# Kernel optimization log

Measured on AMD Instinct MI355X. Metric: run time of the kernel, lower is better.

## Reference

```python
import jax, jax.numpy as jnp
import numpy as np

HID = 384
KV = 384
HEADS = 2
LAYERS = 2
KFFN = 9
WIN = 0.2
SIGMA = 0.3
EPS = 1e-5
HDIM = HID // HEADS


def _sin_pos(T, dim):
    # fairseq SinusoidalPositionalEmbedding; inputs are nonzero floats so all
    # positions are "non-pad": positions = arange(T) + padding_idx + 1 = 1..T
    pos = jnp.arange(1, T + 1, dtype=jnp.float32)
    half = dim // 2
    freqs = jnp.exp(-np.log(10000.0) / (half - 1) * jnp.arange(half, dtype=jnp.float32))
    ang = pos[:, None] * freqs[None, :]
    return jnp.concatenate([jnp.sin(ang), jnp.cos(ang)], axis=-1)  # [T, dim]


def _ln(x, g, b):
    m = jnp.mean(x, axis=-1, keepdims=True)
    v = jnp.var(x, axis=-1, keepdims=True)
    return (x - m) * jax.lax.rsqrt(v + EPS) * g + b


def _window_mask(T1, T2):
    # per-query sliding window over keys (vectorized form of the Python loop)
    w = int(T2 * WIN) // 2
    t = jnp.arange(T1)
    c = (t * T2) // T1                      # win_center = int(t/T1*T2)
    lo = jnp.maximum(0, c - w)
    j = jnp.arange(T2)
    allowed = (j[None, :] >= lo[:, None]) & (j[None, :] < (c + w)[:, None])
    return ~allowed                          # True = masked out, [T1, T2]


def _forward(x1, x2, pos_alpha, ln1_g, ln1_b, qw, kw, vw, ow,
             ln2_g, ln2_b, cw, cb, lw, lb, lnf_g, lnf_b):
    B, T1, C = x1.shape
    T2 = x2.shape[1]
    # no padding (random-normal inputs never have zero abs-sum rows), so all
    # nonpadding multiplies are identity and key_padding_mask is a no-op.
    x1 = x1 + pos_alpha * _sin_pos(T1, C)[None]
    x2 = x2 + pos_alpha * _sin_pos(T2, KV)[None]

    mask = _window_mask(T1, T2)              # [T1, T2] bool
    scaling = HDIM ** -0.5
    guided_loss = jnp.float32(0.0)
    # guided attention mask (lengths == full lengths, no padding)
    ti = jnp.arange(T1, dtype=jnp.float32)[:, None] / T1
    sj = jnp.arange(T2, dtype=jnp.float32)[None, :] / T2
    gmask = 1.0 - jnp.exp(-((sj - ti) ** 2) / (2.0 * SIGMA ** 2))  # [T1, T2]

    aw = None
    for i in range(LAYERS):
        residual = x1
        qn = _ln(x1, ln1_g[i], ln1_b[i])
        q = jnp.einsum('btc,dc->btd', qn, qw[i]) * scaling
        k = jnp.einsum('bsc,dc->bsd', x2, kw[i])
        v = jnp.einsum('bsc,dc->bsd', x2, vw[i])
        q = q.reshape(B, T1, HEADS, HDIM)
        k = k.reshape(B, T2, HEADS, HDIM)
        v = v.reshape(B, T2, HEADS, HDIM)
        scores = jnp.einsum('bqhd,bkhd->bhqk', q, k)
        scores = jnp.where(mask[None, None], jnp.float32(-1e9), scores)
        p = jax.nn.softmax(scores, axis=-1)                  # [B,H,T1,T2]
        attn = jnp.einsum('bhqk,bkhd->bqhd', p, v).reshape(B, T1, C)
        attn = jnp.einsum('btc,dc->btd', attn, ow[i])
        x1 = residual + attn
        if i == 0:  # num_guided_layers = 1
            aw = p.mean(axis=1)                              # head-avg [B,T1,T2]
            guided_loss = guided_loss + (aw * gmask[None]).mean()
        # FFN: Conv1d(C->4C, k=9, SAME) * k^-0.5 -> gelu -> Linear(4C->C)
        residual = x1
        y = _ln(x1, ln2_g[i], ln2_b[i])
        yt = jnp.transpose(y, (0, 2, 1))                     # [B,C,T1]
        h = jax.lax.conv_general_dilated(yt, cw[i], (1,), 'SAME',
                                         dimension_numbers=('NCH', 'OIH', 'NCH'))
        h = (h + cb[i][None, :, None]) * (KFFN ** -0.5)
        h = jax.nn.gelu(jnp.transpose(h, (0, 2, 1)), approximate=False)  # [B,T1,4C]
        y = jnp.einsum('btf,cf->btc', h, lw[i]) + lb[i]
        x1 = residual + y

    x1 = _ln(x1, lnf_g, lnf_b)
    return x1, guided_loss


def setup_inputs() -> dict:
    key = jax.random.key(0)
    ks = jax.random.split(key, 16)
    s = 0.02
    B, T1, T2 = 8, 2048, 512
    return {
        'x1': jax.random.normal(ks[0], (B, T1, HID), jnp.float32),
        'x2': jax.random.normal(ks[1], (B, T2, KV), jnp.float32),
        'pos_alpha': jnp.float32(1.0),
        'ln1_g': jnp.ones((LAYERS, HID), jnp.float32),
        'ln1_b': jnp.zeros((LAYERS, HID), jnp.float32),
        'qw': jax.random.normal(ks[2], (LAYERS, HID, HID), jnp.float32) * s,
        'kw': jax.random.normal(ks[3], (LAYERS, HID, KV), jnp.float32) * s,
        'vw': jax.random.normal(ks[4], (LAYERS, HID, KV), jnp.float32) * s,
        'ow': jax.random.normal(ks[5], (LAYERS, HID, HID), jnp.float32) * s,
        'ln2_g': jnp.ones((LAYERS, HID), jnp.float32),
        'ln2_b': jnp.zeros((LAYERS, HID), jnp.float32),
        'cw': jax.random.normal(ks[6], (LAYERS, 4 * HID, HID, KFFN), jnp.float32) * s,
        'cb': jnp.zeros((LAYERS, 4 * HID), jnp.float32),
        'lw': jax.random.normal(ks[7], (LAYERS, HID, 4 * HID), jnp.float32) * s,
        'lb': jnp.zeros((LAYERS, HID), jnp.float32),
        'lnf_g': jnp.ones((HID,), jnp.float32),
        'lnf_b': jnp.zeros((HID,), jnp.float32),
    }


def reference(x1, x2, pos_alpha, ln1_g, ln1_b, qw, kw, vw, ow,
              ln2_g, ln2_b, cw, cb, lw, lb, lnf_g, lnf_b):
    return _forward(x1, x2, pos_alpha, ln1_g, ln1_b, qw, kw, vw, ow,
                    ln2_g, ln2_b, cw, cb, lw, lb, lnf_g, lnf_b)
```

## Files before the change

### kernel.cpp

```cpp
#include <hip/hip_runtime.h>
#include <math.h>

#define NB 8
#define NT1 2048
#define NT2 512
#define NC 384
#define ND 192
#define NF 1536
#define NKI 3456
#define TPAD 2056

typedef __attribute__((ext_vector_type(8))) short bf16x8;
typedef __attribute__((ext_vector_type(4))) float f32x4;

#define GLOAD16(gsrc, ldst) \
  __builtin_amdgcn_global_load_lds((const __attribute__((address_space(1))) void*)(gsrc), \
                                   (__attribute__((address_space(3))) void*)(ldst), 16, 0, 0)

static __device__ __forceinline__ unsigned short f2bf(float f) {
  unsigned int u = __float_as_uint(f);
  unsigned int r = (u + 0x7fffu + ((u >> 16) & 1u)) >> 16;
  return (unsigned short)r;
}

static __device__ __forceinline__ float warp_sum(float v) {
#pragma unroll
  for (int off = 32; off > 0; off >>= 1) v += __shfl_xor(v, off);
  return v;
}

__global__ __launch_bounds__(256) void k_add_pos2(const float* __restrict__ x,
    const float* __restrict__ alpha_p, float* __restrict__ y, int T, int total2) {
  int i = blockIdx.x * 256 + threadIdx.x;
  if (i >= total2) return;
  int j = i % 192;
  int row = i / 192;
  int t = row % T;
  float freq = __expf(-0.0482216773f * (float)j);
  float ang = (float)(t + 1) * freq;
  float sn, cs;
  __sincosf(ang, &sn, &cs);
  float a = alpha_p[0];
  size_t base = (size_t)row * NC;
  y[base + j] = x[base + j] + a * sn;
  y[base + j + 192] = x[base + j + 192] + a * cs;
}

__global__ __launch_bounds__(256) void k_add_pos2_bf16(const float* __restrict__ x,
    const float* __restrict__ alpha_p, unsigned short* __restrict__ y, int T, int total2) {
  int i = blockIdx.x * 256 + threadIdx.x;
  if (i >= total2) return;
  int j = i % 192;
  int row = i / 192;
  int t = row % T;
  float freq = __expf(-0.0482216773f * (float)j);
  float ang = (float)(t + 1) * freq;
  float sn, cs;
  __sincosf(ang, &sn, &cs);
  float a = alpha_p[0];
  size_t base = (size_t)row * NC;
  y[base + j] = f2bf(x[base + j] + a * sn);
  y[base + j + 192] = f2bf(x[base + j + 192] + a * cs);
}

__global__ __launch_bounds__(256) void k_ln(const float* __restrict__ x,
    const float* __restrict__ g, const float* __restrict__ b,
    float* __restrict__ y, int nrows) {
  int row = blockIdx.x * 4 + (threadIdx.x >> 6);
  int lane = threadIdx.x & 63;
  if (row >= nrows) return;
  const float* xr = x + (size_t)row * NC;
  float v[6];
  float s = 0.f, s2 = 0.f;
#pragma unroll
  for (int i = 0; i < 6; ++i) {
    float t = xr[lane + 64 * i];
    v[i] = t; s += t; s2 += t * t;
  }
  s = warp_sum(s); s2 = warp_sum(s2);
  float mean = s * (1.f / NC);
  float var = s2 * (1.f / NC) - mean * mean;
  float rs = rsqrtf(var + 1e-5f);
  float* yr = y + (size_t)row * NC;
#pragma unroll
  for (int i = 0; i < 6; ++i) {
    int cc = lane + 64 * i;
    yr[cc] = (v[i] - mean) * rs * g[cc] + b[cc];
  }
}

__global__ __launch_bounds__(256) void k_ln_bf16(const float* __restrict__ x,
    const float* __restrict__ g, const float* __restrict__ b,
    unsigned short* __restrict__ y) {
  int row = blockIdx.x * 4 + (threadIdx.x >> 6);
  int lane = threadIdx.x & 63;
  const float* xr = x + (size_t)row * NC;
  float v[6];
  float s = 0.f, s2 = 0.f;
#pragma unroll
  for (int i = 0; i < 6; ++i) {
    float t = xr[lane + 64 * i];
    v[i] = t; s += t; s2 += t * t;
  }
  s = warp_sum(s); s2 = warp_sum(s2);
  float mean = s * (1.f / NC);
  float var = s2 * (1.f / NC) - mean * mean;
  float rs = rsqrtf(var + 1e-5f);
  unsigned short* yr = y + (size_t)row * NC;
#pragma unroll
  for (int i = 0; i < 6; ++i) {
    int cc = lane + 64 * i;
    yr[cc] = f2bf((v[i] - mean) * rs * g[cc] + b[cc]);
  }
}

__global__ __launch_bounds__(256) void k_ln_bf16p(const float* __restrict__ x,
    const float* __restrict__ g, const float* __restrict__ b,
    unsigned short* __restrict__ ypad) {
  int row = blockIdx.x * 4 + (threadIdx.x >> 6);
  int lane = threadIdx.x & 63;
  const float* xr = x + (size_t)row * NC;
  float v[6];
  float s = 0.f, s2 = 0.f;
#pragma unroll
  for (int i = 0; i < 6; ++i) {
    float t = xr[lane + 64 * i];
    v[i] = t; s += t; s2 += t * t;
  }
  s = warp_sum(s); s2 = warp_sum(s2);
  float mean = s * (1.f / NC);
  float var = s2 * (1.f / NC) - mean * mean;
  float rs = rsqrtf(var + 1e-5f);
  int bb = row >> 11, t = row & 2047;
  unsigned short* yr = ypad + ((size_t)(bb * TPAD + t + 4)) * NC;
#pragma unroll
  for (int i = 0; i < 6; ++i) {
    int cc = lane + 64 * i;
    yr[cc] = f2bf((v[i] - mean) * rs * g[cc] + b[cc]);
  }
}

__global__ __launch_bounds__(256) void k_zero_guard(unsigned short* __restrict__ ypad) {
  int i = blockIdx.x * 256 + threadIdx.x;
  if (i >= 24576) return;
  int c = i % NC;
  int r = (i / NC) % 8;
  int b = i / (NC * 8);
  int t = (r < 4) ? r : (2048 + r);
  ypad[((size_t)b * TPAD + t) * NC + c] = 0;
}

__global__ __launch_bounds__(256) void k_pack_cw2(const float* __restrict__ cw,
    unsigned short* __restrict__ cwp) {
  __shared__ float s[NKI];
  int f = blockIdx.x;
  const float* src = cw + (size_t)f * NKI;
  for (int i = threadIdx.x; i < NKI; i += 256) s[i] = src[i];
  __syncthreads();
  unsigned short* dst = cwp + (size_t)f * NKI;
  for (int i = threadIdx.x; i < NKI; i += 256) {
    int kk = i / NC, cc = i - kk * NC;
    dst[i] = f2bf(s[cc * 9 + kk]);
  }
}

__global__ __launch_bounds__(256) void k_cvt_qkvo(const float* __restrict__ qw,
    const float* __restrict__ kw, const float* __restrict__ vw,
    const float* __restrict__ ow, unsigned short* __restrict__ dst, float qscale) {
  int i = blockIdx.x * 256 + threadIdx.x;
  if (i >= 4 * 294912) return;
  int w = i / 294912;
  int j = i - w * 294912;
  const float* s = (w == 0) ? qw : (w == 1) ? kw : (w == 2) ? vw : ow;
  float sc = (w == 0) ? qscale : 1.f;
  dst[i] = f2bf(s[j] * sc);
}

__global__ __launch_bounds__(256) void k_cvt(const float* __restrict__ x,
    unsigned short* __restrict__ y, int n) {
  int i = blockIdx.x * 256 + threadIdx.x;
  if (i < n) y[i] = f2bf(x[i]);
}

__global__ __launch_bounds__(256) void k_pgemm_qkv(
    const unsigned short* __restrict__ Aq,
    const unsigned short* __restrict__ Akv,
    const unsigned short* __restrict__ Wq,
    const unsigned short* __restrict__ Wk,
    const unsigned short* __restrict__ Wv,
    unsigned short* __restrict__ Qb,
    unsigned short* __restrict__ Kb,
    unsigned short* __restrict__ Vtb) {
  __shared__ unsigned short As[128 * 32];
  __shared__ unsigned short Bs[128 * 32];
  const int y = blockIdx.y;
  const int which = (y < 128) ? 0 : (y < 160) ? 1 : 2;
  const unsigned short* A = (which == 0) ? Aq : Akv;
  const unsigned short* W = (which == 0) ? Wq : (which == 1) ? Wk : Wv;
  const int bm = ((which == 0) ? y : (which == 1) ? (y - 128) : (y - 160)) * 128;
  const int bn = blockIdx.x * 128;
  const int tid = threadIdx.x;
  const int lane = tid & 63, wv = tid >> 6;
  const int wr = (wv >> 1) * 64, wc = (wv & 1) * 64;
  f32x4 acc[4][4] = {};

  const int chunk = wv * 2;
  const int rloc = chunk * 16 + (lane >> 2);
  const int slot = (lane & 3) << 3;
  const size_t abase = ((size_t)(bm + rloc)) * NC + slot;
  const size_t bbase = ((size_t)(bn + rloc)) * NC + slot;
  unsigned short* AsW0 = &As[chunk * 512];
  unsigned short* AsW1 = &As[(chunk + 1) * 512];
  unsigned short* BsW0 = &Bs[chunk * 512];
  unsigned short* BsW1 = &Bs[(chunk + 1) * 512];

  const int rsel = lane & 15, ksel = (lane >> 4) * 8;

  for (int kt = 0; kt < NC; kt += 32) {
    GLOAD16(A + abase + kt, AsW0);
    GLOAD16(A + abase + kt + (size_t)16 * NC, AsW1);
    GLOAD16(W + bbase + kt, BsW0);
    GLOAD16(W + bbase + kt + (size_t)16 * NC, BsW1);
    __syncthreads();
    bf16x8 af[4], bfr[4];
#pragma unroll
    for (int m = 0; m < 4; ++m)
      af[m] = *(const bf16x8*)&As[(wr + m * 16 + rsel) * 32 + ksel];
#pragma unroll
    for (int n = 0; n < 4; ++n)
      bfr[n] = *(const bf16x8*)&Bs[(wc + n * 16 + rsel) * 32 + ksel];
#pragma unroll
    for (int m = 0; m < 4; ++m)
#pragma unroll
      for (int n = 0; n < 4; ++n)
        acc[m][n] = __builtin_amdgcn_mfma_f32_16x16x32_bf16(af[m], bfr[n], acc[m][n], 0, 0, 0);
    __syncthreads();
  }

  const int col0 = bn + wc + (lane & 15);
  const int row0 = bm + wr + (lane >> 4) * 4;
#pragma unroll
  for (int m = 0; m < 4; ++m) {
#pragma unroll
    for (int n = 0; n < 4; ++n) {
      int col = col0 + n * 16;
#pragma unroll
      for (int r = 0; r < 4; ++r) {
        int row = row0 + m * 16 + r;
        unsigned short bv = f2bf(acc[m][n][r]);
        if (which == 0) {
          Qb[(size_t)row * NC + col] = bv;
        } else if (which == 1) {
          Kb[(size_t)row * NC + col] = bv;
        } else {
          Vtb[((size_t)((row >> 9) * 384 + col)) * 512 + (row & 511)] = bv;
        }
      }
    }
  }
}

__global__ __launch_bounds__(256) void k_pgemm_o(
    const unsigned short* __restrict__ A,
    const unsigned short* __restrict__ W,
    float* __restrict__ Cf) {
  __shared__ unsigned short As[128 * 32];
  __shared__ unsigned short Bs[128 * 32];
  const int bn = blockIdx.x * 128;
  const int bm = blockIdx.y * 128;
  const int tid = threadIdx.x;
  const int lane = tid & 63, wv = tid >> 6;
  const int wr = (wv >> 1) * 64, wc = (wv & 1) * 64;
  f32x4 acc[4][4] = {};

  const int chunk = wv * 2;
  const int rloc = chunk * 16 + (lane >> 2);
  const int slot = (lane & 3) << 3;
  const size_t abase = ((size_t)(bm + rloc)) * NC + slot;
  const size_t bbase = ((size_t)(bn + rloc)) * NC + slot;
  unsigned short* AsW0 = &As[chunk * 512];
  unsigned short* AsW1 = &As[(chunk + 1) * 512];
  unsigned short* BsW0 = &Bs[chunk * 512];
  unsigned short* BsW1 = &Bs[(chunk + 1) * 512];

  const int rsel = lane & 15, ksel = (lane >> 4) * 8;

  for (int kt = 0; kt < NC; kt += 32) {
    GLOAD16(A + abase + kt, AsW0);
    GLOAD16(A + abase + kt + (size_t)16 * NC, AsW1);
    GLOAD16(W + bbase + kt, BsW0);
    GLOAD16(W + bbase + kt + (size_t)16 * NC, BsW1);
    __syncthreads();
    bf16x8 af[4], bfr[4];
#pragma unroll
    for (int m = 0; m < 4; ++m)
      af[m] = *(const bf16x8*)&As[(wr + m * 16 + rsel) * 32 + ksel];
#pragma unroll
    for (int n = 0; n < 4; ++n)
      bfr[n] = *(const bf16x8*)&Bs[(wc + n * 16 + rsel) * 32 + ksel];
#pragma unroll
    for (int m = 0; m < 4; ++m)
#pragma unroll
      for (int n = 0; n < 4; ++n)
        acc[m][n] = __builtin_amdgcn_mfma_f32_16x16x32_bf16(af[m], bfr[n], acc[m][n], 0, 0, 0);
    __syncthreads();
  }

  const int col0 = bn + wc + (lane & 15);
  const int row0 = bm + wr + (lane >> 4) * 4;
#pragma unroll
  for (int m = 0; m < 4; ++m) {
#pragma unroll
    for (int n = 0; n < 4; ++n) {
      int col = col0 + n * 16;
#pragma unroll
      for (int r = 0; r < 4; ++r) {
        int row = row0 + m * 16 + r;
        size_t oi = (size_t)row * NC + col;
        Cf[oi] = acc[m][n][r] + Cf[oi];
      }
    }
  }
}

__global__ __launch_bounds__(512) void k_conv_mfma(
    const unsigned short* __restrict__ Ypad,
    const unsigned short* __restrict__ Wp,
    const float* __restrict__ cb,
    unsigned short* __restrict__ H) {
  __shared__ unsigned short As[2][256 * 64];
  __shared__ unsigned short Bs[2][128 * 64];
  const int bm = blockIdx.x * 256;
  const int bn = blockIdx.y * 128;
  const int b = bm >> 11, t0 = bm & 2047;
  const int tid = threadIdx.x;
  const int lane = tid & 63, wv = tid >> 6;
  const int wvM = wv >> 1, wvN = wv & 1;
  const int rsel = lane & 15, ghi = lane >> 4;
  const int l8 = lane >> 3, g8 = lane & 7;
  const int gsrc = (g8 ^ l8) * 8;

  f32x4 acc[4][4] = {};

  const size_t arow0 = (size_t)(b * TPAD + t0 + wv * 32 + l8);
  const size_t brow0 = (size_t)(bn + wv * 16 + l8);

#define CONV_STAGE(T, DB)                                                     \
  {                                                                           \
    const int kt_ = (T) * 64;                                                 \
    const int kk_ = kt_ / NC;                                                 \
    const int c0_ = kt_ - kk_ * NC;                                           \
    const size_t asrc_ = (arow0 + kk_) * NC + c0_ + gsrc;                     \
    GLOAD16(Ypad + asrc_, &As[DB][(wv * 32) * 64]);                           \
    GLOAD16(Ypad + asrc_ + (size_t)8 * NC, &As[DB][(wv * 32 + 8) * 64]);      \
    GLOAD16(Ypad + asrc_ + (size_t)16 * NC, &As[DB][(wv * 32 + 16) * 64]);    \
    GLOAD16(Ypad + asrc_ + (size_t)24 * NC, &As[DB][(wv * 32 + 24) * 64]);    \
    const size_t bsrc_ = brow0 * NKI + kt_ + gsrc;                            \
    GLOAD16(Wp + bsrc_, &Bs[DB][(wv * 16) * 64]);                             \
    GLOAD16(Wp + bsrc_ + (size_t)8 * NKI, &Bs[DB][(wv * 16 + 8) * 64]);       \
  }

  CONV_STAGE(0, 0);
  CONV_STAGE(1, 1);
  asm volatile("s_waitcnt vmcnt(6)" ::: "memory");
  __builtin_amdgcn_sched_barrier(0);
  __builtin_amdgcn_s_barrier();

  const int arow = wvM * 64;
  const int brow = wvN * 64;
  int db = 0;
  for (int t = 0; t < 54; ++t) {
    bf16x8 af[4][2], bfr[4][2];
#pragma unroll
    for (int m = 0; m < 4; ++m) {
      int r = arow + m * 16 + rsel;
#pragma unroll
      for (int k = 0; k < 2; ++k)
        af[m][k] = *(const bf16x8*)&As[db][r * 64 + (((k * 4 + ghi) ^ (r & 7)) * 8)];
    }
#pragma unroll
    for (int n = 0; n < 4; ++n) {
      int r = brow + n * 16 + rsel;
#pragma unroll
      for (int k = 0; k < 2; ++k)
        bfr[n][k] = *(const bf16x8*)&Bs[db][r * 64 + (((k * 4 + ghi) ^ (r & 7)) * 8)];
    }
    __builtin_amdgcn_s_setprio(1);
#pragma unroll
    for (int m = 0; m < 4; ++m)
#pragma unroll
      for (int n = 0; n < 4; ++n)
        acc[m][n] = __builtin_amdgcn_mfma_f32_16x16x32_bf16(af[m][0], bfr[n][0], acc[m][n], 0, 0, 0);
    __builtin_amdgcn_s_setprio(0);
    __builtin_amdgcn_sched_barrier(0);
    asm volatile("s_waitcnt lgkmcnt(0)" ::: "memory");
    __builtin_amdgcn_sched_barrier(0);
    __builtin_amdgcn_s_barrier();
    if (t + 2 < 54) CONV_STAGE(t + 2, db);
    __builtin_amdgcn_s_setprio(1);
#pragma unroll
    for (int m = 0; m < 4; ++m)
#pragma unroll
      for (int n = 0; n < 4; ++n)
        acc[m][n] = __builtin_amdgcn_mfma_f32_16x16x32_bf16(af[m][1], bfr[n][1], acc[m][n], 0, 0, 0);
    __builtin_amdgcn_s_setprio(0);
    __builtin_amdgcn_sched_barrier(0);
    if (t + 2 < 54) {
      asm volatile("s_waitcnt vmcnt(6)" ::: "memory");
    } else {
      asm volatile("s_waitcnt vmcnt(0)" ::: "memory");
    }
    __builtin_amdgcn_sched_barrier(0);
    __builtin_amdgcn_s_barrier();
    db ^= 1;
  }
#undef CONV_STAGE

  const int col0 = bn + wvN * 64 + rsel;
  const int row0 = bm + wvM * 64 + ghi * 4;
#pragma unroll
  for (int m = 0; m < 4; ++m) {
#pragma unroll
    for (int n = 0; n < 4; ++n) {
      int col = col0 + n * 16;
      float cbv = cb[col];
#pragma unroll
      for (int r = 0; r < 4; ++r) {
        int row = row0 + m * 16 + r;
        float xv = (acc[m][n][r] + cbv) * 0.33333333333333333f;
        float ge = 0.5f * xv * (1.f + erff(xv * 0.70710678118654752f));
        H[(size_t)row * NF + col] = f2bf(ge);
      }
    }
  }
}

__global__ __launch_bounds__(256) void k_lin_mfma(
    const unsigned short* __restrict__ H,
    const unsigned short* __restrict__ Wb,
    const float* __restrict__ lb,
    float* __restrict__ x1a) {
  __shared__ unsigned short As[128 * 32];
  __shared__ unsigned short Bs[128 * 32];
  const int bn = blockIdx.x * 128;
  const int bm = blockIdx.y * 128;
  const int tid = threadIdx.x;
  const int lane = tid & 63, wv = tid >> 6;
  const int wr = (wv >> 1) * 64, wc = (wv & 1) * 64;
  f32x4 acc[4][4] = {};

  const int chunk = wv * 2;
  const int rloc = chunk * 16 + (lane >> 2);
  const int slot = (lane & 3) << 3;
  const size_t abase = ((size_t)(bm + rloc)) * NF + slot;
  const size_t bbase = ((size_t)(bn + rloc)) * NF + slot;
  unsigned short* AsW0 = &As[chunk * 512];
  unsigned short* AsW1 = &As[(chunk + 1) * 512];
  unsigned short* BsW0 = &Bs[chunk * 512];
  unsigned short* BsW1 = &Bs[(chunk + 1) * 512];

  const int rsel = lane & 15, ksel = (lane >> 4) * 8;

  for (int kt = 0; kt < NF; kt += 32) {
    GLOAD16(H + abase + kt, AsW0);
    GLOAD16(H + abase + kt + (size_t)16 * NF, AsW1);
    GLOAD16(Wb + bbase + kt, BsW0);
    GLOAD16(Wb + bbase + kt + (size_t)16 * NF, BsW1);
    __syncthreads();
    bf16x8 af[4], bfr[4];
#pragma unroll
    for (int m = 0; m < 4; ++m)
      af[m] = *(const bf16x8*)&As[(wr + m * 16 + rsel) * 32 + ksel];
#pragma unroll
    for (int n = 0; n < 4; ++n)
      bfr[n] = *(const bf16x8*)&Bs[(wc + n * 16 + rsel) * 32 + ksel];
#pragma unroll
    for (int m = 0; m < 4; ++m)
#pragma unroll
      for (int n = 0; n < 4; ++n)
        acc[m][n] = __builtin_amdgcn_mfma_f32_16x16x32_bf16(af[m], bfr[n], acc[m][n], 0, 0, 0);
    __syncthreads();
  }

  const int col0 = bn + wc + (lane & 15);
  const int row0 = bm + wr + (lane >> 4) * 4;
#pragma unroll
  for (int m = 0; m < 4; ++m) {
#pragma unroll
    for (int n = 0; n < 4; ++n) {
      int col = col0 + n * 16;
      float lbv = lb[col];
#pragma unroll
      for (int r = 0; r < 4; ++r) {
        int row = row0 + m * 16 + r;
        size_t oi = (size_t)row * NC + col;
        x1a[oi] = acc[m][n][r] + lbv + x1a[oi];
      }
    }
  }
}

__global__ __launch_bounds__(256) void k_attn_mfma(
    const unsigned short* __restrict__ qbb,
    const unsigned short* __restrict__ kbb,
    const unsigned short* __restrict__ vtb,
    unsigned short* __restrict__ o, int guided, float* __restrict__ gl) {
  __shared__ unsigned short lds[32768];
  const int tid = threadIdx.x;
  const int lane = tid & 63, wv = tid >> 6;
  const int rsel = lane & 15, ghi = lane >> 4;
  const int idx = blockIdx.x;
  const int tg = idx & 31;
  const int bh = idx >> 5;
  const int h = bh & 1, b = bh >> 1;
  const int t0 = tg * 64;
  const int c0 = t0 >> 2;
  int klo = c0 - 51; if (klo < 0) klo = 0;
  klo &= ~7;
  if (klo > 384) klo = 384;

  const unsigned short* qrow = qbb + (size_t)(b * NT1 + t0 + wv * 16 + rsel) * NC + h * ND;
  bf16x8 qf[6];
#pragma unroll
  for (int kk = 0; kk < 6; ++kk)
    qf[kk] = *(const bf16x8*)(qrow + kk * 32 + ghi * 8);

  {
    const size_t kbase = (size_t)(b * NT2 + klo) * NC + h * ND;
#pragma unroll
    for (int it = 0; it < 12; ++it) {
      int g = it * 256 + tid;
      int row = g / 24, go = g % 24;
      int gs = go ^ (row & 7);
      GLOAD16(kbb + kbase + (size_t)row * NC + gs * 8, &lds[(it * 256 + wv * 64) * 8]);
    }
  }
  __syncthreads();

  f32x4 accs[8] = {};
#pragma unroll
  for (int kk = 0; kk < 6; ++kk) {
#pragma unroll
    for (int n = 0; n < 8; ++n) {
      int row = n * 16 + rsel;
      bf16x8 bfr = *(const bf16x8*)&lds[row * 192 + (((kk * 4 + ghi) ^ (rsel & 7)) * 8)];
      accs[n] = __builtin_amdgcn_mfma_f32_16x16x32_bf16(qf[kk], bfr, accs[n], 0, 0, 0);
    }
  }

  unsigned short* pl = &lds[24576 + wv * 2048];
  float gacc = 0.f;
  const int t0w = t0 + wv * 16;
#pragma unroll
  for (int r = 0; r < 4; ++r) {
    int t = t0w + ghi * 4 + r;
    int c = t >> 2;
    int loq = c - 51; if (loq < 0) loq = 0;
    int hiq = c + 51; if (hiq > NT2) hiq = NT2;
    float sv[8];
    float mx = -1e30f;
#pragma unroll
    for (int n = 0; n < 8; ++n) {
      int j = klo + n * 16 + rsel;
      float s = (j >= loq && j < hiq) ? accs[n][r] : -1e30f;
      sv[n] = s; mx = fmaxf(mx, s);
    }
#pragma unroll
    for (int off = 1; off < 16; off <<= 1) mx = fmaxf(mx, __shfl_xor(mx, off));
    float e[8]; float se = 0.f;
#pragma unroll
    for (int n = 0; n < 8; ++n) { e[n] = __expf(sv[n] - mx); se += e[n]; }
#pragma unroll
    for (int off = 1; off < 16; off <<= 1) se += __shfl_xor(se, off);
    float inv = 1.f / se;
    int q = ghi * 4 + r;
#pragma unroll
    for (int n = 0; n < 8; ++n) {
      float pv = e[n] * inv;
      int klocal = n * 16 + rsel;
      pl[q * 128 + (((klocal >> 3) ^ (q & 7)) * 8) + (klocal & 7)] = f2bf(pv);
      if (guided) {
        int j = klo + klocal;
        float d = (float)j * (1.f / NT2) - (float)t * (1.f / NT1);
        gacc += pv * (1.f - __expf(-(d * d) * 5.5555555556f));
      }
    }
  }
  if (guided) {
    gacc = warp_sum(gacc);
    if (lane == 0) atomicAdd(gl, gacc * (1.f / 16777216.f));
  }
  __syncthreads();

  {
    const size_t vbase = ((size_t)(b * 2 + h) * ND) * NT2 + klo;
#pragma unroll
    for (int it = 0; it < 12; ++it) {
      int g = it * 256 + tid;
      int row = g >> 4, go = g & 15;
      int gs = go ^ (row & 7);
      GLOAD16(vtb + vbase + (size_t)row * NT2 + gs * 8, &lds[(it * 256 + wv * 64) * 8]);
    }
  }
  __syncthreads();

  f32x4 acco[12] = {};
#pragma unroll
  for (int kt = 0; kt < 4; ++kt) {
    bf16x8 pa = *(const bf16x8*)&pl[rsel * 128 + (((kt * 4 + ghi) ^ (rsel & 7)) * 8)];
#pragma unroll
    for (int n = 0; n < 12; ++n) {
      int row = n * 16 + rsel;
      bf16x8 bfr = *(const bf16x8*)&lds[row * 128 + (((kt * 4 + ghi) ^ (rsel & 7)) * 8)];
      acco[n] = __builtin_amdgcn_mfma_f32_16x16x32_bf16(pa, bfr, acco[n], 0, 0, 0);
    }
  }

  unsigned short* obase = o + (size_t)(b * NT1 + t0w + ghi * 4) * NC + h * ND;
#pragma unroll
  for (int n = 0; n < 12; ++n) {
#pragma unroll
    for (int r = 0; r < 4; ++r) {
      obase[(size_t)r * NC + n * 16 + rsel] = f2bf(acco[n][r]);
    }
  }
}

extern "C" void kernel_launch(void* const* d_in, const int* in_sizes, int n_in,
                              void* d_out, int out_size, void* d_ws, size_t ws_size,
                              hipStream_t stream) {
  (void)in_sizes; (void)n_in; (void)out_size; (void)ws_size;
  const float* x1    = (const float*)d_in[0];
  const float* x2    = (const float*)d_in[1];
  const float* alpha = (const float*)d_in[2];
  const float* ln1_g = (const float*)d_in[3];
  const float* ln1_b = (const float*)d_in[4];
  const float* qw    = (const float*)d_in[5];
  const float* kw    = (const float*)d_in[6];
  const float* vw    = (const float*)d_in[7];
  const float* ow    = (const float*)d_in[8];
  const float* ln2_g = (const float*)d_in[9];
  const float* ln2_b = (const float*)d_in[10];
  const float* cw    = (const float*)d_in[11];
  const float* cb    = (const float*)d_in[12];
  const float* lw    = (const float*)d_in[13];
  const float* lb    = (const float*)d_in[14];
  const float* lnf_g = (const float*)d_in[15];
  const float* lnf_b = (const float*)d_in[16];
  float* out = (float*)d_out;
  float* gl = out + 6291456;

  float* p = (float*)d_ws;
  float* x1a = p; p += 6291456;
  unsigned short* us = (unsigned short*)p;
  unsigned short* x2b  = us; us += 1572864;
  unsigned short* tmpb = us; us += 6291456;
  unsigned short* ypad = us; us += 8 * TPAD * NC;
  unsigned short* cwpb = us; us += 2 * (size_t)NF * NKI;
  unsigned short* lwb  = us; us += 2 * (size_t)NC * NF;
  unsigned short* hb   = us; us += (size_t)16384 * NF;
  unsigned short* qbb  = us; us += 6291456;
  unsigned short* kbb  = us; us += 1572864;
  unsigned short* vtb  = us; us += 1572864;
  unsigned short* qwb  = us; us += 294912;
  unsigned short* kwb  = us; us += 294912;
  unsigned short* vwb  = us; us += 294912;
  unsigned short* owb  = us; us += 294912;

  hipMemsetAsync(gl, 0, sizeof(float), stream);
  k_zero_guard<<<96, 256, 0, stream>>>(ypad);
  k_add_pos2<<<12288, 256, 0, stream>>>(x1, alpha, x1a, NT1, 3145728);
  k_add_pos2_bf16<<<3072, 256, 0, stream>>>(x2, alpha, x2b, NT2, 786432);

  const float scaling = 0.07216878364870323f;
  k_cvt_qkvo<<<4608, 256, 0, stream>>>(qw, kw, vw, ow, qwb, scaling);
  k_cvt<<<4608, 256, 0, stream>>>(lw, lwb, 1179648);
  k_pack_cw2<<<3072, 256, 0, stream>>>(cw, cwpb);

  for (int l = 0; l < 2; ++l) {
    k_ln_bf16<<<4096, 256, 0, stream>>>(x1a, ln1_g + l * 384, ln1_b + l * 384, tmpb);
    k_pgemm_qkv<<<dim3(3, 192), 256, 0, stream>>>(tmpb, x2b,
        qwb + (size_t)l * 147456, kwb + (size_t)l * 147456, vwb + (size_t)l * 147456,
        qbb, kbb, vtb);
    k_attn_mfma<<<512, 256, 0, stream>>>(qbb, kbb, vtb, tmpb, l == 0 ? 1 : 0, gl);
    k_pgemm_o<<<dim3(3, 128), 256, 0, stream>>>(tmpb, owb + (size_t)l * 147456, x1a);
    k_ln_bf16p<<<4096, 256, 0, stream>>>(x1a, ln2_g + l * 384, ln2_b + l * 384, ypad);
    k_conv_mfma<<<dim3(64, 12), 512, 0, stream>>>(ypad, cwpb + (size_t)l * 5308416, cb + l * 1536, hb);
    k_lin_mfma<<<dim3(3, 128), 256, 0, stream>>>(hb, lwb + (size_t)l * 589824, lb + l * 384, x1a);
  }
  k_ln<<<4096, 256, 0, stream>>>(x1a, lnf_g, lnf_b, out, 16384);
}
```

Baseline: 673.9 us.

## Share a double-buffered swizzled GEMM mainloop across QKV, O and linear kernels

Moves the three 128x128 bf16 GEMM kernels (QKV projection, output projection, FFN linear) onto one shared mainloop. It uses BK=64, double-buffered LDS with async global-to-LDS loads issued two tiles ahead, and an XOR-swizzled LDS layout to avoid bank conflicts. MFMA bursts are split in two halves around the barrier, with s_setprio raised during compute. The aim is to hide global load latency and halve the barriers per K step, at the cost of 4x more LDS per block, which may lower occupancy.

```diff
diff --git a/kernel.cpp b/kernel.cpp
--- a/kernel.cpp
+++ b/kernel.cpp
@@ -182,6 +182,90 @@
   if (i < n) y[i] = f2bf(x[i]);
 }
 
+static __device__ __forceinline__ void gemm128_db(
+    const unsigned short* __restrict__ A,
+    const unsigned short* __restrict__ W,
+    int K, int ntiles, int bm, int bn,
+    unsigned short* AsB, unsigned short* BsB,
+    f32x4 (&acc)[4][4]) {
+  const int tid = threadIdx.x;
+  const int lane = tid & 63, wv = tid >> 6;
+  const int rsel = lane & 15, ghi = lane >> 4;
+  const int l8 = lane >> 3, g8 = lane & 7;
+  const int gsrc = (g8 ^ l8) * 8;
+  const size_t abase = (size_t)(bm + wv * 32 + l8) * K + gsrc;
+  const size_t bbase = (size_t)(bn + wv * 32 + l8) * K + gsrc;
+
+#define GDB_STAGE(T, DB)                                                        \
+  {                                                                             \
+    const size_t k_ = (size_t)(T) * 64;                                         \
+    GLOAD16(A + abase + k_, AsB + (DB) * 8192 + (wv * 32) * 64);                \
+    GLOAD16(A + abase + k_ + (size_t)8 * K, AsB + (DB) * 8192 + (wv * 32 + 8) * 64);   \
+    GLOAD16(A + abase + k_ + (size_t)16 * K, AsB + (DB) * 8192 + (wv * 32 + 16) * 64); \
+    GLOAD16(A + abase + k_ + (size_t)24 * K, AsB + (DB) * 8192 + (wv * 32 + 24) * 64); \
+    GLOAD16(W + bbase + k_, BsB + (DB) * 8192 + (wv * 32) * 64);                \
+    GLOAD16(W + bbase + k_ + (size_t)8 * K, BsB + (DB) * 8192 + (wv * 32 + 8) * 64);   \
+    GLOAD16(W + bbase + k_ + (size_t)16 * K, BsB + (DB) * 8192 + (wv * 32 + 16) * 64); \
+    GLOAD16(W + bbase + k_ + (size_t)24 * K, BsB + (DB) * 8192 + (wv * 32 + 24) * 64); \
+  }
+
+  GDB_STAGE(0, 0);
+  GDB_STAGE(1, 1);
+  asm volatile("s_waitcnt vmcnt(8)" ::: "memory");
+  __builtin_amdgcn_sched_barrier(0);
+  __builtin_amdgcn_s_barrier();
+
+  const int arow = (wv >> 1) * 64;
+  const int brow = (wv & 1) * 64;
+  int db = 0;
+  for (int t = 0; t < ntiles; ++t) {
+    bf16x8 af[4][2], bfr[4][2];
+#pragma unroll
+    for (int m = 0; m < 4; ++m) {
+      int r = arow + m * 16 + rsel;
+#pragma unroll
+      for (int k = 0; k < 2; ++k)
+        af[m][k] = *(const bf16x8*)&AsB[db * 8192 + r * 64 + (((k * 4 + ghi) ^ (r & 7)) * 8)];
+    }
+#pragma unroll
+    for (int n = 0; n < 4; ++n) {
+      int r = brow + n * 16 + rsel;
+#pragma unroll
+      for (int k = 0; k < 2; ++k)
+        bfr[n][k] = *(const bf16x8*)&BsB[db * 8192 + r * 64 + (((k * 4 + ghi) ^ (r & 7)) * 8)];
+    }
+    __builtin_amdgcn_s_setprio(1);
+#pragma unroll
+    for (int m = 0; m < 4; ++m)
+#pragma unroll
+      for (int n = 0; n < 4; ++n)
+        acc[m][n] = __builtin_amdgcn_mfma_f32_16x16x32_bf16(af[m][0], bfr[n][0], acc[m][n], 0, 0, 0);
+    __builtin_amdgcn_s_setprio(0);
+    __builtin_amdgcn_sched_barrier(0);
+    asm volatile("s_waitcnt lgkmcnt(0)" ::: "memory");
+    __builtin_amdgcn_sched_barrier(0);
+    __builtin_amdgcn_s_barrier();
+    if (t + 2 < ntiles) GDB_STAGE(t + 2, db);
+    __builtin_amdgcn_s_setprio(1);
+#pragma unroll
+    for (int m = 0; m < 4; ++m)
+#pragma unroll
+      for (int n = 0; n < 4; ++n)
+        acc[m][n] = __builtin_amdgcn_mfma_f32_16x16x32_bf16(af[m][1], bfr[n][1], acc[m][n], 0, 0, 0);
+    __builtin_amdgcn_s_setprio(0);
+    __builtin_amdgcn_sched_barrier(0);
+    if (t + 2 < ntiles) {
+      asm volatile("s_waitcnt vmcnt(8)" ::: "memory");
+    } else {
+      asm volatile("s_waitcnt vmcnt(0)" ::: "memory");
+    }
+    __builtin_amdgcn_sched_barrier(0);
+    __builtin_amdgcn_s_barrier();
+    db ^= 1;
+  }
+#undef GDB_STAGE
+}
+
 __global__ __launch_bounds__(256) void k_pgemm_qkv(
     const unsigned short* __restrict__ Aq,
     const unsigned short* __restrict__ Akv,
@@ -191,54 +275,20 @@
     unsigned short* __restrict__ Qb,
     unsigned short* __restrict__ Kb,
     unsigned short* __restrict__ Vtb) {
-  __shared__ unsigned short As[128 * 32];
-  __shared__ unsigned short Bs[128 * 32];
+  __shared__ unsigned short As[2 * 8192];
+  __shared__ unsigned short Bs[2 * 8192];
   const int y = blockIdx.y;
   const int which = (y < 128) ? 0 : (y < 160) ? 1 : 2;
   const unsigned short* A = (which == 0) ? Aq : Akv;
   const unsigned short* W = (which == 0) ? Wq : (which == 1) ? Wk : Wv;
   const int bm = ((which == 0) ? y : (which == 1) ? (y - 128) : (y - 160)) * 128;
   const int bn = blockIdx.x * 128;
-  const int tid = threadIdx.x;
-  const int lane = tid & 63, wv = tid >> 6;
-  const int wr = (wv >> 1) * 64, wc = (wv & 1) * 64;
   f32x4 acc[4][4] = {};
-
-  const int chunk = wv * 2;
-  const int rloc = chunk * 16 + (lane >> 2);
-  const int slot = (lane & 3) << 3;
-  const size_t abase = ((size_t)(bm + rloc)) * NC + slot;
-  const size_t bbase = ((size_t)(bn + rloc)) * NC + slot;
-  unsigned short* AsW0 = &As[chunk * 512];
-  unsigned short* AsW1 = &As[(chunk + 1) * 512];
-  unsigned short* BsW0 = &Bs[chunk * 512];
-  unsigned short* BsW1 = &Bs[(chunk + 1) * 512];
-
-  const int rsel = lane & 15, ksel = (lane >> 4) * 8;
-
-  for (int kt = 0; kt < NC; kt += 32) {
-    GLOAD16(A + abase + kt, AsW0);
-    GLOAD16(A + abase + kt + (size_t)16 * NC, AsW1);
-    GLOAD16(W + bbase + kt, BsW0);
-    GLOAD16(W + bbase + kt + (size_t)16 * NC, BsW1);
-    __syncthreads();
-    bf16x8 af[4], bfr[4];
-#pragma unroll
-    for (int m = 0; m < 4; ++m)
-      af[m] = *(const bf16x8*)&As[(wr + m * 16 + rsel) * 32 + ksel];
-#pragma unroll
-    for (int n = 0; n < 4; ++n)
-      bfr[n] = *(const bf16x8*)&Bs[(wc + n * 16 + rsel) * 32 + ksel];
-#pragma unroll
-    for (int m = 0; m < 4; ++m)
-#pragma unroll
-      for (int n = 0; n < 4; ++n)
-        acc[m][n] = __builtin_amdgcn_mfma_f32_16x16x32_bf16(af[m], bfr[n], acc[m][n], 0, 0, 0);
-    __syncthreads();
-  }
-
-  const int col0 = bn + wc + (lane & 15);
-  const int row0 = bm + wr + (lane >> 4) * 4;
+  gemm128_db(A, W, NC, 6, bm, bn, As, Bs, acc);
+
+  const int lane = threadIdx.x & 63, wv = threadIdx.x >> 6;
+  const int col0 = bn + (wv & 1) * 64 + (lane & 15);
+  const int row0 = bm + (wv >> 1) * 64 + (lane >> 4) * 4;
 #pragma unroll
   for (int m = 0; m < 4; ++m) {
 #pragma unroll
@@ -264,50 +314,16 @@
     const unsigned short* __restrict__ A,
     const unsigned short* __restrict__ W,
     float* __restrict__ Cf) {
-  __shared__ unsigned short As[128 * 32];
-  __shared__ unsigned short Bs[128 * 32];
+  __shared__ unsigned short As[2 * 8192];
+  __shared__ unsigned short Bs[2 * 8192];
   const int bn = blockIdx.x * 128;
   const int bm = blockIdx.y * 128;
-  const int tid = threadIdx.x;
-  const int lane = tid & 63, wv = tid >> 6;
-  const int wr = (wv >> 1) * 64, wc = (wv & 1) * 64;
   f32x4 acc[4][4] = {};
-
-  const int chunk = wv * 2;
-  const int rloc = chunk * 16 + (lane >> 2);
-  const int slot = (lane & 3) << 3;
-  const size_t abase = ((size_t)(bm + rloc)) * NC + slot;
-  const size_t bbase = ((size_t)(bn + rloc)) * NC + slot;
-  unsigned short* AsW0 = &As[chunk * 512];
-  unsigned short* AsW1 = &As[(chunk + 1) * 512];
-  unsigned short* BsW0 = &Bs[chunk * 512];
-  unsigned short* BsW1 = &Bs[(chunk + 1) * 512];
-
-  const int rsel = lane & 15, ksel = (lane >> 4) * 8;
-
-  for (int kt = 0; kt < NC; kt += 32) {
-    GLOAD16(A + abase + kt, AsW0);
-    GLOAD16(A + abase + kt + (size_t)16 * NC, AsW1);
-    GLOAD16(W + bbase + kt, BsW0);
-    GLOAD16(W + bbase + kt + (size_t)16 * NC, BsW1);
-    __syncthreads();
-    bf16x8 af[4], bfr[4];
-#pragma unroll
-    for (int m = 0; m < 4; ++m)
-      af[m] = *(const bf16x8*)&As[(wr + m * 16 + rsel) * 32 + ksel];
-#pragma unroll
-    for (int n = 0; n < 4; ++n)
-      bfr[n] = *(const bf16x8*)&Bs[(wc + n * 16 + rsel) * 32 + ksel];
-#pragma unroll
-    for (int m = 0; m < 4; ++m)
-#pragma unroll
-      for (int n = 0; n < 4; ++n)
-        acc[m][n] = __builtin_amdgcn_mfma_f32_16x16x32_bf16(af[m], bfr[n], acc[m][n], 0, 0, 0);
-    __syncthreads();
-  }
-
-  const int col0 = bn + wc + (lane & 15);
-  const int row0 = bm + wr + (lane >> 4) * 4;
+  gemm128_db(A, W, NC, 6, bm, bn, As, Bs, acc);
+
+  const int lane = threadIdx.x & 63, wv = threadIdx.x >> 6;
+  const int col0 = bn + (wv & 1) * 64 + (lane & 15);
+  const int row0 = bm + (wv >> 1) * 64 + (lane >> 4) * 4;
 #pragma unroll
   for (int m = 0; m < 4; ++m) {
 #pragma unroll
@@ -318,6 +334,37 @@
         int row = row0 + m * 16 + r;
         size_t oi = (size_t)row * NC + col;
         Cf[oi] = acc[m][n][r] + Cf[oi];
+      }
+    }
+  }
+}
+
+__global__ __launch_bounds__(256) void k_lin_mfma(
+    const unsigned short* __restrict__ H,
+    const unsigned short* __restrict__ Wb,
+    const float* __restrict__ lb,
+    float* __restrict__ x1a) {
+  __shared__ unsigned short As[2 * 8192];
+  __shared__ unsigned short Bs[2 * 8192];
+  const int bn = blockIdx.x * 128;
+  const int bm = blockIdx.y * 128;
+  f32x4 acc[4][4] = {};
+  gemm128_db(H, Wb, NF, 24, bm, bn, As, Bs, acc);
+
+  const int lane = threadIdx.x & 63, wv = threadIdx.x >> 6;
+  const int col0 = bn + (wv & 1) * 64 + (lane & 15);
+  const int row0 = bm + (wv >> 1) * 64 + (lane >> 4) * 4;
+#pragma unroll
+  for (int m = 0; m < 4; ++m) {
+#pragma unroll
+    for (int n = 0; n < 4; ++n) {
+      int col = col0 + n * 16;
+      float lbv = lb[col];
+#pragma unroll
+      for (int r = 0; r < 4; ++r) {
+        int row = row0 + m * 16 + r;
+        size_t oi = (size_t)row * NC + col;
+        x1a[oi] = acc[m][n][r] + lbv + x1a[oi];
       }
     }
   }
@@ -430,71 +477,6 @@
         float xv = (acc[m][n][r] + cbv) * 0.33333333333333333f;
         float ge = 0.5f * xv * (1.f + erff(xv * 0.70710678118654752f));
         H[(size_t)row * NF + col] = f2bf(ge);
-      }
-    }
-  }
-}
-
-__global__ __launch_bounds__(256) void k_lin_mfma(
-    const unsigned short* __restrict__ H,
-    const unsigned short* __restrict__ Wb,
-    const float* __restrict__ lb,
-    float* __restrict__ x1a) {
-  __shared__ unsigned short As[128 * 32];
-  __shared__ unsigned short Bs[128 * 32];
-  const int bn = blockIdx.x * 128;
-  const int bm = blockIdx.y * 128;
-  const int tid = threadIdx.x;
-  const int lane = tid & 63, wv = tid >> 6;
-  const int wr = (wv >> 1) * 64, wc = (wv & 1) * 64;
-  f32x4 acc[4][4] = {};
-
-  const int chunk = wv * 2;
-  const int rloc = chunk * 16 + (lane >> 2);
-  const int slot = (lane & 3) << 3;
-  const size_t abase = ((size_t)(bm + rloc)) * NF + slot;
-  const size_t bbase = ((size_t)(bn + rloc)) * NF + slot;
-  unsigned short* AsW0 = &As[chunk * 512];
-  unsigned short* AsW1 = &As[(chunk + 1) * 512];
-  unsigned short* BsW0 = &Bs[chunk * 512];
-  unsigned short* BsW1 = &Bs[(chunk + 1) * 512];
-
-  const int rsel = lane & 15, ksel = (lane >> 4) * 8;
-
-  for (int kt = 0; kt < NF; kt += 32) {
-    GLOAD16(H + abase + kt, AsW0);
-    GLOAD16(H + abase + kt + (size_t)16 * NF, AsW1);
-    GLOAD16(Wb + bbase + kt, BsW0);
-    GLOAD16(Wb + bbase + kt + (size_t)16 * NF, BsW1);
-    __syncthreads();
-    bf16x8 af[4], bfr[4];
-#pragma unroll
-    for (int m = 0; m < 4; ++m)
-      af[m] = *(const bf16x8*)&As[(wr + m * 16 + rsel) * 32 + ksel];
-#pragma unroll
-    for (int n = 0; n < 4; ++n)
-      bfr[n] = *(const bf16x8*)&Bs[(wc + n * 16 + rsel) * 32 + ksel];
-#pragma unroll
-    for (int m = 0; m < 4; ++m)
-#pragma unroll
-      for (int n = 0; n < 4; ++n)
-        acc[m][n] = __builtin_amdgcn_mfma_f32_16x16x32_bf16(af[m], bfr[n], acc[m][n], 0, 0, 0);
-    __syncthreads();
-  }
-
-  const int col0 = bn + wc + (lane & 15);
-  const int row0 = bm + wr + (lane >> 4) * 4;
-#pragma unroll
-  for (int m = 0; m < 4; ++m) {
-#pragma unroll
-    for (int n = 0; n < 4; ++n) {
-      int col = col0 + n * 16;
-      float lbv = lb[col];
-#pragma unroll
-      for (int r = 0; r < 4; ++r) {
-        int row = row0 + m * 16 + r;
-        size_t oi = (size_t)row * NC + col;
-        x1a[oi] = acc[m][n][r] + lbv + x1a[oi];
       }
     }
   }
```

After: 657.0 us. 1.03x faster.
